# Kernel tuning notes

Hardware: AMD Instinct MI355X
Metric: run time of the kernel (lower is better)

## Reference

```python
import jax, jax.numpy as jnp
import numpy as np

IN_F, OUT_F = 4096, 11008
B, S = 2, 2048

def setup_inputs() -> dict:
    key = jax.random.key(0)
    k1, k2, k3, k4 = jax.random.split(key, 4)
    x = jax.random.normal(k1, (B, S, IN_F), dtype=jnp.float32)
    # int8 quantized weight, stored as int8 buffer [out_features, in_features]
    w8 = jax.random.randint(k2, (OUT_F, IN_F), -128, 128, dtype=jnp.int32).astype(jnp.int8)
    scales = jax.random.normal(k3, (OUT_F,), dtype=jnp.float32)
    bias = jax.random.normal(k4, (1, OUT_F), dtype=jnp.float32)
    return {"input": x, "int8_weights": w8, "scales": scales, "bias": bias}

def reference(input, int8_weights, scales, bias):
    # w8_a16_forward: cast int8 weight to activation dtype, dense GEMM,
    # then per-output-channel scale and bias add.
    w = int8_weights.astype(input.dtype)                 # [OUT_F, IN_F]
    y = jnp.einsum('bsi,oi->bso', input, w)              # [B, S, OUT_F]
    return y * scales + bias                             # scales broadcast over last dim; bias [1, OUT_F]
```

## Files before the change

kernel.cpp:

```cpp
#include <hip/hip_runtime.h>
#include <stdint.h>

#define MM 4096
#define KK 4096
#define NN 11008
#define NK 64

typedef __bf16 bf16;
typedef bf16 bf16x8 __attribute__((ext_vector_type(8)));
typedef float f32x4 __attribute__((ext_vector_type(4)));

static_assert(sizeof(bf16x8) == 16, "bf16x8 must be 16B");

__device__ __forceinline__ void async_ld16(const void* g, void* l) {
  __builtin_amdgcn_global_load_lds(
      (const __attribute__((address_space(1))) uint32_t*)g,
      (__attribute__((address_space(3))) uint32_t*)l,
      16, 0, 0);
}

__global__ __launch_bounds__(256) void cvt_a_kernel(const float* __restrict__ in,
                                                    bf16* __restrict__ out, int n4) {
  int i = blockIdx.x * 256 + threadIdx.x;
  if (i >= n4) return;
  float4 v = ((const float4*)in)[i];
  union { bf16 h[4]; uint2 u; } p;
  p.h[0] = (bf16)v.x; p.h[1] = (bf16)v.y; p.h[2] = (bf16)v.z; p.h[3] = (bf16)v.w;
  ((uint2*)out)[i] = p.u;
}

__global__ __launch_bounds__(256) void cvt_w_kernel(const int* __restrict__ in,
                                                    bf16* __restrict__ out, int n4) {
  int i = blockIdx.x * 256 + threadIdx.x;
  if (i >= n4) return;
  int4 v = ((const int4*)in)[i];
  union { bf16 h[4]; uint2 u; } p;
  p.h[0] = (bf16)(float)v.x; p.h[1] = (bf16)(float)v.y;
  p.h[2] = (bf16)(float)v.z; p.h[3] = (bf16)(float)v.w;
  ((uint2*)out)[i] = p.u;
}

__global__ __launch_bounds__(512, 2) void gemm256_kernel(
    const bf16* __restrict__ A,
    const bf16* __restrict__ W,
    const float* __restrict__ scales,
    const float* __restrict__ bias,
    float* __restrict__ out) {
  extern __shared__ bf16 lds[];
  bf16* LA = lds;
  bf16* LB = lds + 2 * 16384;

  const int tid  = threadIdx.x;
  const int lane = tid & 63;
  const int wave = tid >> 6;
  const int wr   = wave >> 2;
  const int wc   = wave & 3;

  const int flat = blockIdx.y * 16 + blockIdx.x;
  const int swz  = (flat & 7) * 86 + (flat >> 3);
  const int bm   = swz & 15;
  const int bn   = swz >> 4;

  const int t2   = (tid & 32) ? (tid ^ 2) : tid;
  const int srow = tid >> 3;
  const int skel = (t2 & 7) * 8;
  const bf16* gA = A + (size_t)(bm * 256 + srow) * KK + skel;
  const bf16* gW = W + (size_t)(bn * 256 + srow) * KK + skel;

  const int m16  = lane & 15;
  const int kk   = ((lane >> 4) * 8) ^ (((lane >> 2) & 1) * 16);
  const int aRow = wr * 128 + m16;
  const int bRow = wc * 64 + m16;

  f32x4 acc[8][4] = {};

  auto stage_half = [&](const bf16* g, bf16* l) {
    async_ld16(g, l + wave * 512);
    async_ld16(g + (size_t)64 * KK, l + 64 * 64 + wave * 512);
  };
  stage_half(gW,                    LB);
  stage_half(gA,                    LA);
  stage_half(gW + (size_t)128 * KK, LB + 128 * 64);
  stage_half(gA + (size_t)128 * KK, LA + 128 * 64);
  stage_half(gW + 64,               LB + 16384);
  stage_half(gA + 64,               LA + 16384);
  asm volatile("s_waitcnt vmcnt(4)" ::: "memory");
  __builtin_amdgcn_s_barrier();

  for (int c = 0; c < NK; ++c) {
    const int cb = c & 1;
    const bf16* At = LA + cb * 16384;
    const bf16* Wt = LB + cb * 16384;
    bf16* An = LA + (cb ^ 1) * 16384;
    bf16* Bn = LB + (cb ^ 1) * 16384;
    bf16* Ac = LA + cb * 16384;
    bf16* Bc = LB + cb * 16384;
    const size_t k1 = (size_t)(c + 1) * 64;
    const size_t k2 = (size_t)(c + 2) * 64;

    bf16x8 aLo[4][2], aHi[4][2], bLo[2][2], bHi[2][2];

#pragma unroll
    for (int fm = 0; fm < 4; ++fm)
#pragma unroll
      for (int kc = 0; kc < 2; ++kc)
        aLo[fm][kc] = *(const bf16x8*)(At + (aRow + fm * 16) * 64 + kc * 32 + kk);
#pragma unroll
    for (int fn = 0; fn < 2; ++fn)
#pragma unroll
      for (int kc = 0; kc < 2; ++kc)
        bLo[fn][kc] = *(const bf16x8*)(Wt + (bRow + fn * 16) * 64 + kc * 32 + kk);
    if (c + 1 < NK) stage_half(gW + (size_t)128 * KK + k1, Bn + 128 * 64);
    __builtin_amdgcn_s_barrier();
    asm volatile("s_waitcnt lgkmcnt(0)" ::: "memory");
    __builtin_amdgcn_s_setprio(1);
#pragma unroll
    for (int fm = 0; fm < 4; ++fm)
#pragma unroll
      for (int fn = 0; fn < 2; ++fn)
#pragma unroll
        for (int kc = 0; kc < 2; ++kc)
          acc[fm][fn] = __builtin_amdgcn_mfma_f32_16x16x32_bf16(aLo[fm][kc], bLo[fn][kc], acc[fm][fn], 0, 0, 0);
    __builtin_amdgcn_s_setprio(0);
    __builtin_amdgcn_s_barrier();

#pragma unroll
    for (int fn = 0; fn < 2; ++fn)
#pragma unroll
      for (int kc = 0; kc < 2; ++kc)
        bHi[fn][kc] = *(const bf16x8*)(Wt + (bRow + (fn + 2) * 16) * 64 + kc * 32 + kk);
    if (c + 1 < NK) stage_half(gA + (size_t)128 * KK + k1, An + 128 * 64);
    __builtin_amdgcn_s_barrier();
    asm volatile("s_waitcnt lgkmcnt(0)" ::: "memory");
    __builtin_amdgcn_s_setprio(1);
#pragma unroll
    for (int fm = 0; fm < 4; ++fm)
#pragma unroll
      for (int fn = 0; fn < 2; ++fn)
#pragma unroll
        for (int kc = 0; kc < 2; ++kc)
          acc[fm][fn + 2] = __builtin_amdgcn_mfma_f32_16x16x32_bf16(aLo[fm][kc], bHi[fn][kc], acc[fm][fn + 2], 0, 0, 0);
    __builtin_amdgcn_s_setprio(0);
    __builtin_amdgcn_s_barrier();

#pragma unroll
    for (int fm = 0; fm < 4; ++fm)
#pragma unroll
      for (int kc = 0; kc < 2; ++kc)
        aHi[fm][kc] = *(const bf16x8*)(At + (aRow + (fm + 4) * 16) * 64 + kc * 32 + kk);
    if (c + 2 < NK) stage_half(gW + k2, Bc);
    __builtin_amdgcn_s_barrier();
    asm volatile("s_waitcnt lgkmcnt(0)" ::: "memory");
    __builtin_amdgcn_s_setprio(1);
#pragma unroll
    for (int fm = 0; fm < 4; ++fm)
#pragma unroll
      for (int fn = 0; fn < 2; ++fn)
#pragma unroll
        for (int kc = 0; kc < 2; ++kc)
          acc[fm + 4][fn] = __builtin_amdgcn_mfma_f32_16x16x32_bf16(aHi[fm][kc], bLo[fn][kc], acc[fm + 4][fn], 0, 0, 0);
    __builtin_amdgcn_s_setprio(0);
    __builtin_amdgcn_s_barrier();

    if (c + 2 < NK) stage_half(gA + k2, Ac);
    __builtin_amdgcn_s_barrier();
    __builtin_amdgcn_s_setprio(1);
#pragma unroll
    for (int fm = 0; fm < 4; ++fm)
#pragma unroll
      for (int fn = 0; fn < 2; ++fn)
#pragma unroll
        for (int kc = 0; kc < 2; ++kc)
          acc[fm + 4][fn + 2] = __builtin_amdgcn_mfma_f32_16x16x32_bf16(aHi[fm][kc], bHi[fn][kc], acc[fm + 4][fn + 2], 0, 0, 0);
    __builtin_amdgcn_s_setprio(0);
    if (c + 2 < NK) asm volatile("s_waitcnt vmcnt(4)" ::: "memory");
    else            asm volatile("s_waitcnt vmcnt(0)" ::: "memory");
    __builtin_amdgcn_s_barrier();
  }

  const int row0 = bm * 256 + wr * 128 + ((lane >> 4) * 4);
  const int col0 = bn * 256 + wc * 64 + (lane & 15);
#pragma unroll
  for (int fn = 0; fn < 4; ++fn) {
    const int col = col0 + fn * 16;
    const float s = scales[col];
    const float b = bias[col];
#pragma unroll
    for (int fm = 0; fm < 8; ++fm) {
      const int r0 = row0 + fm * 16;
#pragma unroll
      for (int r = 0; r < 4; ++r)
        out[(size_t)(r0 + r) * NN + col] = acc[fm][fn][r] * s + b;
    }
  }
}

__device__ __forceinline__ void epilogue128(f32x4 acc[4][4],
                                            const float* __restrict__ scales,
                                            const float* __restrict__ bias,
                                            float* __restrict__ out,
                                            int bm, int bn, int lane, int wr, int wc) {
  const int row0 = bm * 128 + wr * 64 + ((lane >> 4) * 4);
  const int col0 = bn * 128 + wc * 64 + (lane & 15);
#pragma unroll
  for (int tn = 0; tn < 4; ++tn) {
    const int col = col0 + tn * 16;
    const float s = scales[col];
    const float b = bias[col];
#pragma unroll
    for (int tm = 0; tm < 4; ++tm) {
      const int r0 = row0 + tm * 16;
#pragma unroll
      for (int r = 0; r < 4; ++r)
        out[(long)(r0 + r) * NN + col] = acc[tm][tn][r] * s + b;
    }
  }
}

__global__ __launch_bounds__(256, 2) void gemm_fused_kernel(
    const float* __restrict__ A,
    const int* __restrict__ W32,
    const float* __restrict__ scales,
    const float* __restrict__ bias,
    float* __restrict__ out) {
  __shared__ bf16 As[128 * 32];
  __shared__ bf16 Ws[128 * 32];
  const int tid  = threadIdx.x;
  const int lane = tid & 63;
  const int wave = tid >> 6;
  const int wr   = wave >> 1, wc = wave & 1;
  const int bm   = blockIdx.x, bn = blockIdx.y;

  f32x4 acc[4][4] = {};

  const int r    = tid >> 1;
  const int kk16 = (tid & 1) * 16;

  const float* Ag = A + (long)(bm * 128 + r) * KK + kk16;
  const int*   Wg = W32 + (long)(bn * 128 + r) * KK + kk16;
  bf16* Asw = As + r * 32 + kk16;
  bf16* Wsw = Ws + r * 32 + kk16;

  for (int k0 = 0; k0 < KK; k0 += 32) {
    float4 a0 = *(const float4*)(Ag + k0);
    float4 a1 = *(const float4*)(Ag + k0 + 4);
    float4 a2 = *(const float4*)(Ag + k0 + 8);
    float4 a3 = *(const float4*)(Ag + k0 + 12);
    int4 v0 = *(const int4*)(Wg + k0);
    int4 v1 = *(const int4*)(Wg + k0 + 4);
    int4 v2 = *(const int4*)(Wg + k0 + 8);
    int4 v3 = *(const int4*)(Wg + k0 + 12);
    __syncthreads();
    bf16x8 h0, h1, w0, w1;
    h0[0] = (bf16)a0.x; h0[1] = (bf16)a0.y; h0[2] = (bf16)a0.z; h0[3] = (bf16)a0.w;
    h0[4] = (bf16)a1.x; h0[5] = (bf16)a1.y; h0[6] = (bf16)a1.z; h0[7] = (bf16)a1.w;
    h1[0] = (bf16)a2.x; h1[1] = (bf16)a2.y; h1[2] = (bf16)a2.z; h1[3] = (bf16)a2.w;
    h1[4] = (bf16)a3.x; h1[5] = (bf16)a3.y; h1[6] = (bf16)a3.z; h1[7] = (bf16)a3.w;
    w0[0] = (bf16)(float)v0.x; w0[1] = (bf16)(float)v0.y;
    w0[2] = (bf16)(float)v0.z; w0[3] = (bf16)(float)v0.w;
    w0[4] = (bf16)(float)v1.x; w0[5] = (bf16)(float)v1.y;
    w0[6] = (bf16)(float)v1.z; w0[7] = (bf16)(float)v1.w;
    w1[0] = (bf16)(float)v2.x; w1[1] = (bf16)(float)v2.y;
    w1[2] = (bf16)(float)v2.z; w1[3] = (bf16)(float)v2.w;
    w1[4] = (bf16)(float)v3.x; w1[5] = (bf16)(float)v3.y;
    w1[6] = (bf16)(float)v3.z; w1[7] = (bf16)(float)v3.w;
    *(bf16x8*)(Asw)     = h0;
    *(bf16x8*)(Asw + 8) = h1;
    *(bf16x8*)(Wsw)     = w0;
    *(bf16x8*)(Wsw + 8) = w1;
    __syncthreads();
    const int m16 = lane & 15;
    const int ko  = (lane >> 4) * 8;
    bf16x8 af[4], bg[4];
#pragma unroll
    for (int t = 0; t < 4; ++t) {
      af[t] = *(const bf16x8*)(As + (wr * 64 + t * 16 + m16) * 32 + ko);
      bg[t] = *(const bf16x8*)(Ws + (wc * 64 + t * 16 + m16) * 32 + ko);
    }
#pragma unroll
    for (int tm = 0; tm < 4; ++tm)
#pragma unroll
      for (int tn = 0; tn < 4; ++tn)
        acc[tm][tn] = __builtin_amdgcn_mfma_f32_16x16x32_bf16(af[tm], bg[tn], acc[tm][tn], 0, 0, 0);
  }
  epilogue128(acc, scales, bias, out, bm, bn, lane, wr, wc);
}

extern "C" void kernel_launch(void* const* d_in, const int* in_sizes, int n_in,
                              void* d_out, int out_size, void* d_ws, size_t ws_size,
                              hipStream_t stream) {
  const float* x      = (const float*)d_in[0];
  const int*   w32    = (const int*)d_in[1];
  const float* scales = (const float*)d_in[2];
  const float* bias   = (const float*)d_in[3];
  float*       out    = (float*)d_out;

  const size_t A_BYTES = (size_t)MM * KK * 2;
  const size_t W_BYTES = (size_t)NN * KK * 2;

  if (ws_size >= A_BYTES + W_BYTES) {
    static bool attr_done = false;
    if (!attr_done) {
      (void)hipFuncSetAttribute((const void*)gemm256_kernel,
                                hipFuncAttributeMaxDynamicSharedMemorySize, 131072);
      attr_done = true;
    }
    bf16* A16 = (bf16*)d_ws;
    bf16* W16 = (bf16*)((char*)d_ws + A_BYTES);
    const int na = MM * KK / 4;
    hipLaunchKernelGGL(cvt_a_kernel, dim3((na + 255) / 256), dim3(256), 0, stream, x, A16, na);
    const int nw = NN * KK / 4;
    hipLaunchKernelGGL(cvt_w_kernel, dim3((nw + 255) / 256), dim3(256), 0, stream, w32, W16, nw);
    hipLaunchKernelGGL(gemm256_kernel, dim3(MM / 256, NN / 256), dim3(512), 131072, stream,
                       A16, W16, scales, bias, out);
  } else {
    hipLaunchKernelGGL(gemm_fused_kernel, dim3(MM / 128, NN / 128), dim3(256), 0, stream,
                       x, w32, scales, bias, out);
  }
}
```

Before: 698.6 us.

## Merge GEMM k-step phases into two halves with fewer barriers and peeled tail

Restructures each k-step of the bf16 MFMA GEMM from four load/compute phases into two. All LDS fragment reads for the step (aLo, bLo, bHi, aHi) are hoisted to the start, and global→LDS stages are issued in pairs. This cuts the barriers per iteration from about seven to two. The last two iterations are peeled so the staging and tail conditions become compile-time constants. The intent is to lower synchronization overhead and lengthen the MFMA bursts, at the cost of more live registers for the fragments and less interleaving of loads with compute.

```diff
diff --git a/kernel.cpp b/kernel.cpp
--- a/kernel.cpp
+++ b/kernel.cpp
@@ -78,6 +78,7 @@
     async_ld16(g, l + wave * 512);
     async_ld16(g + (size_t)64 * KK, l + 64 * 64 + wave * 512);
   };
+
   stage_half(gW,                    LB);
   stage_half(gA,                    LA);
   stage_half(gW + (size_t)128 * KK, LB + 128 * 64);
@@ -87,7 +88,7 @@
   asm volatile("s_waitcnt vmcnt(4)" ::: "memory");
   __builtin_amdgcn_s_barrier();
 
-  for (int c = 0; c < NK; ++c) {
+  auto kstep = [&](int c, bool s1, bool s2, bool tail) {
     const int cb = c & 1;
     const bf16* At = LA + cb * 16384;
     const bf16* Wt = LB + cb * 16384;
@@ -110,9 +111,22 @@
 #pragma unroll
       for (int kc = 0; kc < 2; ++kc)
         bLo[fn][kc] = *(const bf16x8*)(Wt + (bRow + fn * 16) * 64 + kc * 32 + kk);
-    if (c + 1 < NK) stage_half(gW + (size_t)128 * KK + k1, Bn + 128 * 64);
-    __builtin_amdgcn_s_barrier();
-    asm volatile("s_waitcnt lgkmcnt(0)" ::: "memory");
+#pragma unroll
+    for (int fn = 0; fn < 2; ++fn)
+#pragma unroll
+      for (int kc = 0; kc < 2; ++kc)
+        bHi[fn][kc] = *(const bf16x8*)(Wt + (bRow + (fn + 2) * 16) * 64 + kc * 32 + kk);
+#pragma unroll
+    for (int fm = 0; fm < 4; ++fm)
+#pragma unroll
+      for (int kc = 0; kc < 2; ++kc)
+        aHi[fm][kc] = *(const bf16x8*)(At + (aRow + (fm + 4) * 16) * 64 + kc * 32 + kk);
+
+    if (s1) {
+      stage_half(gW + (size_t)128 * KK + k1, Bn + 128 * 64);
+      stage_half(gA + (size_t)128 * KK + k1, An + 128 * 64);
+    }
+
     __builtin_amdgcn_s_setprio(1);
 #pragma unroll
     for (int fm = 0; fm < 4; ++fm)
@@ -121,18 +135,6 @@
 #pragma unroll
         for (int kc = 0; kc < 2; ++kc)
           acc[fm][fn] = __builtin_amdgcn_mfma_f32_16x16x32_bf16(aLo[fm][kc], bLo[fn][kc], acc[fm][fn], 0, 0, 0);
-    __builtin_amdgcn_s_setprio(0);
-    __builtin_amdgcn_s_barrier();
-
-#pragma unroll
-    for (int fn = 0; fn < 2; ++fn)
-#pragma unroll
-      for (int kc = 0; kc < 2; ++kc)
-        bHi[fn][kc] = *(const bf16x8*)(Wt + (bRow + (fn + 2) * 16) * 64 + kc * 32 + kk);
-    if (c + 1 < NK) stage_half(gA + (size_t)128 * KK + k1, An + 128 * 64);
-    __builtin_amdgcn_s_barrier();
-    asm volatile("s_waitcnt lgkmcnt(0)" ::: "memory");
-    __builtin_amdgcn_s_setprio(1);
 #pragma unroll
     for (int fm = 0; fm < 4; ++fm)
 #pragma unroll
@@ -141,16 +143,15 @@
         for (int kc = 0; kc < 2; ++kc)
           acc[fm][fn + 2] = __builtin_amdgcn_mfma_f32_16x16x32_bf16(aLo[fm][kc], bHi[fn][kc], acc[fm][fn + 2], 0, 0, 0);
     __builtin_amdgcn_s_setprio(0);
+
+    asm volatile("s_waitcnt lgkmcnt(0)" ::: "memory");
     __builtin_amdgcn_s_barrier();
 
-#pragma unroll
-    for (int fm = 0; fm < 4; ++fm)
-#pragma unroll
-      for (int kc = 0; kc < 2; ++kc)
-        aHi[fm][kc] = *(const bf16x8*)(At + (aRow + (fm + 4) * 16) * 64 + kc * 32 + kk);
-    if (c + 2 < NK) stage_half(gW + k2, Bc);
-    __builtin_amdgcn_s_barrier();
-    asm volatile("s_waitcnt lgkmcnt(0)" ::: "memory");
+    if (s2) {
+      stage_half(gW + k2, Bc);
+      stage_half(gA + k2, Ac);
+    }
+
     __builtin_amdgcn_s_setprio(1);
 #pragma unroll
     for (int fm = 0; fm < 4; ++fm)
@@ -159,12 +160,6 @@
 #pragma unroll
         for (int kc = 0; kc < 2; ++kc)
           acc[fm + 4][fn] = __builtin_amdgcn_mfma_f32_16x16x32_bf16(aHi[fm][kc], bLo[fn][kc], acc[fm + 4][fn], 0, 0, 0);
-    __builtin_amdgcn_s_setprio(0);
-    __builtin_amdgcn_s_barrier();
-
-    if (c + 2 < NK) stage_half(gA + k2, Ac);
-    __builtin_amdgcn_s_barrier();
-    __builtin_amdgcn_s_setprio(1);
 #pragma unroll
     for (int fm = 0; fm < 4; ++fm)
 #pragma unroll
@@ -173,10 +168,15 @@
         for (int kc = 0; kc < 2; ++kc)
           acc[fm + 4][fn + 2] = __builtin_amdgcn_mfma_f32_16x16x32_bf16(aHi[fm][kc], bHi[fn][kc], acc[fm + 4][fn + 2], 0, 0, 0);
     __builtin_amdgcn_s_setprio(0);
-    if (c + 2 < NK) asm volatile("s_waitcnt vmcnt(4)" ::: "memory");
-    else            asm volatile("s_waitcnt vmcnt(0)" ::: "memory");
+
+    if (!tail) asm volatile("s_waitcnt vmcnt(4)" ::: "memory");
+    else       asm volatile("s_waitcnt vmcnt(0)" ::: "memory");
     __builtin_amdgcn_s_barrier();
-  }
+  };
+
+  for (int c = 0; c < NK - 2; ++c) kstep(c, true, true, false);
+  kstep(NK - 2, true, false, true);
+  kstep(NK - 1, false, false, true);
 
   const int row0 = bm * 256 + wr * 128 + ((lane >> 4) * 4);
   const int col0 = bn * 256 + wc * 64 + (lane & 15);
```

After: 685.4 us. Within noise of the previous version (-1.9%).
